# Optimization experiments

Hardware: AMD Instinct MI355X
Metric: run time of the kernel (lower is better)

## Reference

```python
import jax, jax.numpy as jnp
import numpy as np
import math

INPUT_SIZE = 1024
HIDDEN_SIZE = 1024
BATCH = 4096


def setup_inputs() -> dict:
    key = jax.random.key(0)
    ks = jax.random.split(key, 16)
    stddev = 1.0 / math.sqrt(HIDDEN_SIZE)

    def unif(k, shape):
        return jax.random.uniform(k, shape, minval=-stddev, maxval=stddev, dtype=jnp.float32)

    inp = {
        'x': jax.random.normal(ks[0], (BATCH, INPUT_SIZE), dtype=jnp.float32),
        'h_prev': jax.random.normal(ks[1], (BATCH, HIDDEN_SIZE), dtype=jnp.float32),
        'c_prev': jax.random.normal(ks[2], (BATCH, HIDDEN_SIZE), dtype=jnp.float32),
        'igx': unif(ks[3], (INPUT_SIZE, HIDDEN_SIZE)),
        'igu': unif(ks[4], (HIDDEN_SIZE, HIDDEN_SIZE)),
        'ib': unif(ks[5], (HIDDEN_SIZE,)),
        'fgx': unif(ks[6], (INPUT_SIZE, HIDDEN_SIZE)),
        'fgu': unif(ks[7], (HIDDEN_SIZE, HIDDEN_SIZE)),
        'fb': unif(ks[8], (HIDDEN_SIZE,)),
        'ogx': unif(ks[9], (INPUT_SIZE, HIDDEN_SIZE)),
        'ogu': unif(ks[10], (HIDDEN_SIZE, HIDDEN_SIZE)),
        'ob': unif(ks[11], (HIDDEN_SIZE,)),
        'cgx': unif(ks[12], (INPUT_SIZE, HIDDEN_SIZE)),
        'cgu': unif(ks[13], (HIDDEN_SIZE, HIDDEN_SIZE)),
        'cb': unif(ks[14], (HIDDEN_SIZE,)),
    }
    return inp


def reference(x, h_prev, c_prev, igx, igu, ib, fgx, fgu, fb, ogx, ogu, ob, cgx, cgu, cb):
    # Fuse the 8 gate matmuls into 2 GEMMs via concatenated weights.
    # Wx: [input_size, 4H], Wh: [hidden, 4H], b: [4H]; gate order i,f,o,c.
    Wx = jnp.concatenate([igx, fgx, ogx, cgx], axis=1)
    Wh = jnp.concatenate([igu, fgu, ogu, cgu], axis=1)
    b = jnp.concatenate([ib, fb, ob, cb], axis=0)
    gates = x @ Wx + h_prev @ Wh + b  # [B, 4H]
    H = c_prev.shape[-1]
    ig = jax.nn.sigmoid(gates[:, 0 * H:1 * H])
    fg = jax.nn.sigmoid(gates[:, 1 * H:2 * H])
    og = jax.nn.sigmoid(gates[:, 2 * H:3 * H])
    cc = jnp.tanh(gates[:, 3 * H:4 * H])
    c = fg * c_prev + ig * cc
    h = og * jnp.tanh(c)
    return (h, c)
```

## Files before the change

kernel.cpp:

```cpp
#include <hip/hip_runtime.h>
#include <hip/hip_bf16.h>

typedef unsigned short u16;
typedef unsigned int u32;
typedef short bf16x8 __attribute__((ext_vector_type(8)));
typedef float f32x4 __attribute__((ext_vector_type(4)));
typedef u16 u16x8 __attribute__((ext_vector_type(8)));

#define HID 1024
#define BATCH 4096
#define KTOT 2048

__device__ __forceinline__ u16 f2bf(float f) {
  u32 v = __builtin_bit_cast(u32, f);
  u32 r = (v + 0x7fffu + ((v >> 16) & 1u)) >> 16;
  return (u16)r;
}
__device__ __forceinline__ float sigmoid_fast(float x) {
  return 1.0f / (1.0f + __expf(-x));
}
__device__ __forceinline__ float tanh_fast(float x) {
  return 2.0f * sigmoid_fast(2.0f * x) - 1.0f;
}

__global__ __launch_bounds__(256) void prep_xh(
    const float* __restrict__ x, const float* __restrict__ hp,
    u16* __restrict__ xh2) {
  int s = blockIdx.x * 256 + threadIdx.x;
  int lane = s & 63, unit = s >> 6;
  int kstep = unit & 63, rowtile = unit >> 6;
  int m = lane & 15, quad = lane >> 4;
  int row = rowtile * 16 + m;
  int kg = kstep * 32 + quad * 8;
  const float* src = (kg < 1024) ? (x + (size_t)row * 1024 + kg)
                                 : (hp + (size_t)row * 1024 + (kg - 1024));
  f32x4 a = *(const f32x4*)(src);
  f32x4 b = *(const f32x4*)(src + 4);
  u16x8 v;
#pragma unroll
  for (int j = 0; j < 4; ++j) { v[j] = f2bf(a[j]); v[j + 4] = f2bf(b[j]); }
  *(u16x8*)(xh2 + (size_t)s * 8) = v;
}

__global__ __launch_bounds__(256) void prep_w(
    const float* __restrict__ igx, const float* __restrict__ fgx,
    const float* __restrict__ ogx, const float* __restrict__ cgx,
    const float* __restrict__ igu, const float* __restrict__ fgu,
    const float* __restrict__ ogu, const float* __restrict__ cgu,
    u16* __restrict__ bt) {
  __shared__ u16 lds[64 * 66];
  const float* srcs[8] = {igx, fgx, ogx, cgx, igu, fgu, ogu, cgu};
  int bid = blockIdx.x;
  int m = bid >> 8;
  int tile = bid & 255;
  int th = tile & 15, tk = tile >> 4;
  int h0 = th << 6, k0 = tk << 6;
  int g = m & 3, which = m >> 2;
  const float* W = srcs[m] + (size_t)k0 * HID + h0;

  int t = threadIdx.x;

  int r1 = t >> 4;
  int c1 = (t & 15) << 2;
#pragma unroll
  for (int p = 0; p < 4; ++p) {
    int row = (p << 4) + r1;
    f32x4 v = *(const f32x4*)(W + (size_t)row * HID + c1);
    u32 p0 = (u32)f2bf(v[0]) | ((u32)f2bf(v[1]) << 16);
    u32 p1 = (u32)f2bf(v[2]) | ((u32)f2bf(v[3]) << 16);
    u32* d = (u32*)&lds[row * 66 + c1];
    d[0] = p0;
    d[1] = p1;
  }
  __syncthreads();

  int nl = t >> 2;
  int kc = t & 3;
  int np = (((h0 + nl) >> 4) << 6) + (g << 4) + ((h0 + nl) & 15);
  int ntile = np >> 4, m16 = np & 15;
  int kstep = which * 32 + (k0 >> 5);
  size_t unit = (size_t)ntile * 64 + kstep;
  int lane16 = kc * 16 + m16;
  u16x8 a, b;
#pragma unroll
  for (int j = 0; j < 8; ++j) {
    a[j] = lds[(kc * 8 + j) * 66 + nl];
    b[j] = lds[(kc * 8 + 32 + j) * 66 + nl];
  }
  *(u16x8*)(&bt[unit * 512 + lane16 * 8]) = a;
  *(u16x8*)(&bt[(unit + 1) * 512 + lane16 * 8]) = b;
}

#define LOAD_FRAGS(buf, kstep_)                                              \
  {                                                                          \
    int _kk = (kstep_);                                                      \
    af[buf][0]  = *(const bf16x8*)(pA + (size_t)(0 * 64 + _kk) * 512);       \
    bfr[buf][0] = *(const bf16x8*)(pB + (size_t)(0 * 64 + _kk) * 512);       \
    bfr[buf][1] = *(const bf16x8*)(pB + (size_t)(1 * 64 + _kk) * 512);       \
    bfr[buf][2] = *(const bf16x8*)(pB + (size_t)(2 * 64 + _kk) * 512);       \
    bfr[buf][3] = *(const bf16x8*)(pB + (size_t)(3 * 64 + _kk) * 512);       \
    af[buf][1]  = *(const bf16x8*)(pA + (size_t)(1 * 64 + _kk) * 512);       \
    af[buf][2]  = *(const bf16x8*)(pA + (size_t)(2 * 64 + _kk) * 512);       \
    af[buf][3]  = *(const bf16x8*)(pA + (size_t)(3 * 64 + _kk) * 512);       \
  }

#define CONSUME_FRAGS(buf)                                                   \
  {                                                                          \
    _Pragma("unroll") for (int mi = 0; mi < 4; ++mi)                         \
        _Pragma("unroll") for (int ni = 0; ni < 4; ++ni)                     \
            acc[mi][ni] = __builtin_amdgcn_mfma_f32_16x16x32_bf16(           \
                af[buf][mi], bfr[buf][ni], acc[mi][ni], 0, 0, 0);            \
  }

__global__ __launch_bounds__(256, 3) void lstm_gemm(
    const u16* __restrict__ xh2, const u16* __restrict__ bt,
    const float* __restrict__ cprev,
    const float* __restrict__ ib, const float* __restrict__ fb,
    const float* __restrict__ ob, const float* __restrict__ cb,
    float* __restrict__ hout, float* __restrict__ cout) {
  int t = threadIdx.x;
  int brow = blockIdx.x, bcol = blockIdx.y;
  int w = t >> 6, l = t & 63;
  int wr = (w >> 1) * 64;
  int lrow = l & 15, quad = l >> 4;

  f32x4 acc[4][4] = {};
  bf16x8 af[2][4], bfr[2][4];

  const u16* pA = xh2 + ((size_t)(brow * 8 + (w >> 1) * 4) * 64) * 512 + l * 8;
  const u16* pB = bt  + ((size_t)(bcol * 8 + (w & 1) * 4) * 64) * 512 + l * 8;

  LOAD_FRAGS(0, 0)
  for (int kt = 0; kt < 64; kt += 2) {
    LOAD_FRAGS(1, kt + 1)
    CONSUME_FRAGS(0)
    LOAD_FRAGS(0, (kt + 2) & 63)
    CONSUME_FRAGS(1)
  }

  int sb = bcol * 2 + (w & 1);
  int hcol = sb * 16 + lrow;
  float bi = ib[hcol];
  float bff = fb[hcol];
  float bo = ob[hcol];
  float bc = cb[hcol];
  int grow = brow * 128;

#pragma unroll
  for (int mi = 0; mi < 4; ++mi) {
    int row0 = grow + wr + mi * 16 + quad * 4;
#pragma unroll
    for (int r = 0; r < 4; ++r) {
      size_t idx = (size_t)(row0 + r) * HID + hcol;
      float gi = sigmoid_fast(acc[mi][0][r] + bi);
      float gf = sigmoid_fast(acc[mi][1][r] + bff);
      float go = sigmoid_fast(acc[mi][2][r] + bo);
      float gc = tanh_fast(acc[mi][3][r] + bc);
      float cp = cprev[idx];
      float cv = gf * cp + gi * gc;
      float hv = go * tanh_fast(cv);
      hout[idx] = hv;
      cout[idx] = cv;
    }
  }
}

extern "C" void kernel_launch(void* const* d_in, const int* in_sizes, int n_in,
                              void* d_out, int out_size, void* d_ws, size_t ws_size,
                              hipStream_t stream) {
  const float* x   = (const float*)d_in[0];
  const float* hp  = (const float*)d_in[1];
  const float* cp  = (const float*)d_in[2];
  const float* igx = (const float*)d_in[3];
  const float* igu = (const float*)d_in[4];
  const float* ib  = (const float*)d_in[5];
  const float* fgx = (const float*)d_in[6];
  const float* fgu = (const float*)d_in[7];
  const float* fb  = (const float*)d_in[8];
  const float* ogx = (const float*)d_in[9];
  const float* ogu = (const float*)d_in[10];
  const float* ob  = (const float*)d_in[11];
  const float* cgx = (const float*)d_in[12];
  const float* cgu = (const float*)d_in[13];
  const float* cb  = (const float*)d_in[14];

  u16* bt  = (u16*)d_ws;
  u16* xh2 = bt + (size_t)4096 * 2048;
  float* hout = (float*)d_out;
  float* cout = hout + (size_t)BATCH * HID;

  prep_xh<<<4096, 256, 0, stream>>>(x, hp, xh2);
  prep_w<<<2048, 256, 0, stream>>>(igx, fgx, ogx, cgx, igu, fgu, ogu, cgu, bt);
  lstm_gemm<<<dim3(32, 32), 256, 0, stream>>>(xh2, bt, cp, ib, fb, ob, cb,
                                              hout, cout);
}
```

Measured before the change: 220.8 us.

## Use single-wave GEMM blocks with swizzled tile order and pinned MFMA schedule

```diff
diff --git a/kernel.cpp b/kernel.cpp
--- a/kernel.cpp
+++ b/kernel.cpp
@@ -74,21 +74,22 @@
   }
   __syncthreads();
 
-  int nl = t >> 2;
-  int kc = t & 3;
-  int np = (((h0 + nl) >> 4) << 6) + (g << 4) + ((h0 + nl) & 15);
-  int ntile = np >> 4, m16 = np & 15;
-  int kstep = which * 32 + (k0 >> 5);
-  size_t unit = (size_t)ntile * 64 + kstep;
-  int lane16 = kc * 16 + m16;
-  u16x8 a, b;
-#pragma unroll
-  for (int j = 0; j < 8; ++j) {
-    a[j] = lds[(kc * 8 + j) * 66 + nl];
-    b[j] = lds[(kc * 8 + 32 + j) * 66 + nl];
-  }
-  *(u16x8*)(&bt[unit * 512 + lane16 * 8]) = a;
-  *(u16x8*)(&bt[(unit + 1) * 512 + lane16 * 8]) = b;
+  int u = t >> 5;
+  int j = u & 3, ks = u >> 2;
+  int s0 = (t & 31) << 1;
+  int ntile = (((h0 >> 4) + j) << 2) | g;
+  size_t unit = (size_t)ntile * 64 + (size_t)which * 32 + (k0 >> 5) + ks;
+  u16* dst = bt + unit * 512 + (size_t)s0 * 8;
+#pragma unroll
+  for (int p = 0; p < 2; ++p) {
+    int s = s0 + p;
+    int m16 = s & 15, quad = s >> 4;
+    u16x8 v;
+#pragma unroll
+    for (int jj = 0; jj < 8; ++jj)
+      v[jj] = lds[(ks * 32 + quad * 8 + jj) * 66 + (j << 4) + m16];
+    *(u16x8*)(dst + p * 8) = v;
+  }
 }
 
 #define LOAD_FRAGS(buf, kstep_)                                              \
@@ -112,43 +113,48 @@
                 af[buf][mi], bfr[buf][ni], acc[mi][ni], 0, 0, 0);            \
   }
 
-__global__ __launch_bounds__(256, 3) void lstm_gemm(
+#define SCHED_PIN()                                                          \
+  __builtin_amdgcn_sched_group_barrier(0x020, 8, 0);       \
+  __builtin_amdgcn_sched_group_barrier(0x008, 16, 0);
+
+__global__ __launch_bounds__(64) void lstm_gemm(
     const u16* __restrict__ xh2, const u16* __restrict__ bt,
     const float* __restrict__ cprev,
     const float* __restrict__ ib, const float* __restrict__ fb,
     const float* __restrict__ ob, const float* __restrict__ cb,
     float* __restrict__ hout, float* __restrict__ cout) {
-  int t = threadIdx.x;
-  int brow = blockIdx.x, bcol = blockIdx.y;
-  int w = t >> 6, l = t & 63;
-  int wr = (w >> 1) * 64;
+  int l = threadIdx.x;
+  int bid = blockIdx.x;
+  int bcol = ((bid & 7) << 3) | ((bid >> 3) & 7);
+  int brow = bid >> 6;
   int lrow = l & 15, quad = l >> 4;
 
   f32x4 acc[4][4] = {};
   bf16x8 af[2][4], bfr[2][4];
 
-  const u16* pA = xh2 + ((size_t)(brow * 8 + (w >> 1) * 4) * 64) * 512 + l * 8;
-  const u16* pB = bt  + ((size_t)(bcol * 8 + (w & 1) * 4) * 64) * 512 + l * 8;
+  const u16* pA = xh2 + ((size_t)(brow * 4) * 64) * 512 + l * 8;
+  const u16* pB = bt  + ((size_t)(bcol * 4) * 64) * 512 + l * 8;
 
   LOAD_FRAGS(0, 0)
   for (int kt = 0; kt < 64; kt += 2) {
     LOAD_FRAGS(1, kt + 1)
     CONSUME_FRAGS(0)
+    SCHED_PIN()
     LOAD_FRAGS(0, (kt + 2) & 63)
     CONSUME_FRAGS(1)
-  }
-
-  int sb = bcol * 2 + (w & 1);
-  int hcol = sb * 16 + lrow;
+    SCHED_PIN()
+  }
+
+  int hcol = bcol * 16 + lrow;
   float bi = ib[hcol];
   float bff = fb[hcol];
   float bo = ob[hcol];
   float bc = cb[hcol];
-  int grow = brow * 128;
+  int grow = brow * 64;
 
 #pragma unroll
   for (int mi = 0; mi < 4; ++mi) {
-    int row0 = grow + wr + mi * 16 + quad * 4;
+    int row0 = grow + mi * 16 + quad * 4;
 #pragma unroll
     for (int r = 0; r < 4; ++r) {
       size_t idx = (size_t)(row0 + r) * HID + hcol;
@@ -191,6 +197,5 @@
 
   prep_xh<<<4096, 256, 0, stream>>>(x, hp, xh2);
   prep_w<<<2048, 256, 0, stream>>>(igx, fgx, ogx, cgx, igu, fgu, ogu, cgu, bt);
-  lstm_gemm<<<dim3(32, 32), 256, 0, stream>>>(xh2, bt, cp, ib, fb, ob, cb,
-                                              hout, cout);
-}
+  lstm_gemm<<<4096, 64, 0, stream>>>(xh2, bt, cp, ib, fb, ob, cb, hout, cout);
+}
```

After: 231.3 us. 1.05x slower.
